# Kernel optimization log

Hardware: AMD Instinct MI355X
Metric: run time of the kernel (lower is better)

## Reference

```python
import jax, jax.numpy as jnp
import numpy as np

BLOCK = 256


def setup_inputs() -> dict:
    key = jax.random.key(0)
    ks = jax.random.split(key, 6)
    b, n, hid = 2, 4096, 2048
    h, d = 16, 128
    x = jax.random.normal(ks[0], (b, n, hid), dtype=jnp.float32)
    slope_rate = jax.random.uniform(ks[1], (h, 1, 1), dtype=jnp.float32)
    Wqkv = jax.random.normal(ks[2], (3 * h * d, hid), dtype=jnp.float32) * 0.02
    Wg = jax.random.normal(ks[3], (h * d, hid), dtype=jnp.float32) * 0.02
    norm_w = jnp.ones((h * d,), dtype=jnp.float32)
    Wo = jax.random.normal(ks[4], (hid, h * d), dtype=jnp.float32) * 0.02
    return {"x": x, "slope_rate": slope_rate, "Wqkv": Wqkv, "Wg": Wg, "norm_w": norm_w, "Wo": Wo}


def reference(x, slope_rate, Wqkv, Wg, norm_w, Wo):
    b, n, hid = x.shape
    h = slope_rate.shape[0]
    d = Wqkv.shape[0] // (3 * h)
    nb = n // BLOCK

    qkv = jax.nn.silu(x @ Wqkv.T).reshape(b, n, h, 3 * d)
    q, k, v = jnp.split(qkv, 3, axis=-1)           # each (b, n, h, d)
    # -> (b, h, n, d)
    q = q.transpose(0, 2, 1, 3)
    k = k.transpose(0, 2, 1, 3)
    v = v.transpose(0, 2, 1, 3)

    s = slope_rate.astype(jnp.float32)             # (h, 1, 1)
    arr = jnp.arange(1, BLOCK + 1, dtype=jnp.float32)
    q_decay = jnp.exp(-s * arr[:, None])           # (h, BLOCK, 1)
    k_decay = jnp.exp(-s * (BLOCK - arr[:, None])) # (h, BLOCK, 1)
    idx = arr[:, None] - arr[None, :]              # (BLOCK, BLOCK)
    diag_decay = jnp.where(idx >= 0, jnp.exp(-s * idx), 0.0)  # (h, BLOCK, BLOCK)
    block_decay = jnp.exp(-s * BLOCK)              # (h, 1, 1)

    # chunk into blocks: (nb, b, h, BLOCK, d)
    def chunk(t):
        return t.reshape(b, h, nb, BLOCK, d).transpose(2, 0, 1, 3, 4)
    qc, kc, vc = chunk(q), chunk(k), chunk(v)

    def step(kv, qkv_blk):
        qi, ki, vi = qkv_blk
        # inter-block: decayed query against running kv state
        out_nd = jnp.einsum('bhmd,bhde->bhme', qi * q_decay, kv)
        # intra-block: decay-masked quadratic attention
        qk = jnp.einsum('bhmd,bhnd->bhmn', qi, ki) * diag_decay
        out_d = jnp.einsum('bhmn,bhne->bhme', qk, vi)
        kv_new = block_decay * kv + jnp.einsum('bhmd,bhme->bhde', ki * k_decay, vi)
        return kv_new, out_nd + out_d

    kv0 = jnp.zeros((b, h, d, d), dtype=jnp.float32)
    _, out_blocks = jax.lax.scan(step, kv0, (qc, kc, vc))  # (nb, b, h, BLOCK, d)

    out = out_blocks.transpose(1, 2, 0, 3, 4).reshape(b, h, n, d)
    out = out.transpose(0, 2, 1, 3).reshape(b, n, h * d)  # b n (h d)

    # RMSNorm
    eps = jnp.finfo(jnp.float32).eps
    rms = jax.lax.rsqrt(jnp.mean(out * out, axis=-1, keepdims=True) + eps)
    out = out * rms * norm_w

    gate = jax.nn.sigmoid(x @ Wg.T)
    return (gate * out) @ Wo.T
```

## Files before the change

### kernel.cpp

```cpp
#include <hip/hip_runtime.h>
#include <stdint.h>

typedef __attribute__((ext_vector_type(8))) short short8;
typedef __attribute__((ext_vector_type(4))) float f32x4;

#define DEV static __device__ __forceinline__

DEV float b2f(unsigned short u) {
  unsigned x = ((unsigned)u) << 16;
  return __builtin_bit_cast(float, x);
}
DEV unsigned short f2b(float f) {
  unsigned x = __builtin_bit_cast(unsigned, f);
  return (unsigned short)((x + 0x7fffu + ((x >> 16) & 1u)) >> 16);
}
DEV void gload16(const unsigned short* g, unsigned short* l) {
  __builtin_amdgcn_global_load_lds((const __attribute__((address_space(1))) void*)g,
                                   (__attribute__((address_space(3))) void*)l, 16, 0, 0);
}
#define MFMA(a, b, c) __builtin_amdgcn_mfma_f32_16x16x32_bf16(a, b, c, 0, 0, 0)
#define BARRIER                          \
  asm volatile("" ::: "memory");         \
  __builtin_amdgcn_s_barrier();          \
  asm volatile("" ::: "memory")

__global__ void k_f2b(const float* __restrict__ in, unsigned short* __restrict__ out, long n) {
  long i = ((long)blockIdx.x * blockDim.x + threadIdx.x) * 4;
  long stride = (long)gridDim.x * blockDim.x * 4;
  for (; i < n; i += stride) {
    float4 f = *(const float4*)(in + i);
    ushort4 o;
    o.x = f2b(f.x); o.y = f2b(f.y); o.z = f2b(f.z); o.w = f2b(f.w);
    *(ushort4*)(out + i) = o;
  }
}

template <int MODE>
__global__ __launch_bounds__(512, 2) void k_gemm(
    const unsigned short* __restrict__ A, const unsigned short* __restrict__ B0,
    const unsigned short* __restrict__ B1,
    unsigned short* __restrict__ o_q, unsigned short* __restrict__ o_k,
    unsigned short* __restrict__ o_v, unsigned short* __restrict__ o_g,
    float* __restrict__ o_f) {
  const int K = 2048, NT = 32;
  __shared__ unsigned short sm[65536];
  int tid = threadIdx.x, w = tid >> 6, lane = tid & 63;
  int wm = w >> 2, wn = w & 3;
  int l15 = lane & 15, l4 = lane >> 4;
  int xcd = blockIdx.x & 7, sub = blockIdx.x >> 3;
  int tm = xcd * 4 + (sub & 3), tn = sub >> 2;
  int brow = tm << 8, bcol = tn << 8;
  const unsigned short* Ab = A + (size_t)brow * K;
  const unsigned short* Bb = (MODE == 1 || bcol < 6144) ? (B0 + (size_t)bcol * K)
                                                        : (B1 + (size_t)(bcol - 6144) * K);
  f32x4 acc[8][4];
#pragma unroll
  for (int m = 0; m < 8; m++)
#pragma unroll
    for (int n = 0; n < 4; n++) acc[m][n] = (f32x4)0.f;

  int rdA[4][2], rdB[4][2];
  const int bslot = (wn >> 1) ? 3 : 1;
  const int bposb = (wn & 1) * 64;
#pragma unroll
  for (int fi = 0; fi < 4; ++fi) {
#pragma unroll
    for (int ks = 0; ks < 2; ++ks) {
      int posA = wm * 64 + fi * 16 + l15;
      rdA[fi][ks] = posA * 128 + (((ks * 4 + l4) ^ (posA & 7)) << 4);
      int posB = bposb + fi * 16 + l15;
      rdB[fi][ks] = bslot * 16384 + posB * 128 + (((ks * 4 + l4) ^ (posB & 7)) << 4);
    }
  }
  const unsigned short* gP[4][2];
  int dL[4][2];
#pragma unroll
  for (int s = 0; s < 4; ++s) {
#pragma unroll
    for (int i = 0; i < 2; ++i) {
      int c = i * 512 + tid;
      int pos = c >> 3, pb = c & 7;
      const unsigned short* gb = (s & 1) ? Bb : Ab;
      int ro = (s >> 1) << 7;
      gP[s][i] = gb + (size_t)(ro + pos) * K + ((pb ^ (pos & 7)) << 3);
      dL[s][i] = s * 16384 + c * 16;
    }
  }

  auto stage = [&](int s, int tgl) {
#pragma unroll
    for (int i = 0; i < 2; ++i) {
      gload16(gP[s][i], (unsigned short*)((char*)sm + (dL[s][i] + tgl)));
      gP[s][i] += 64;
    }
  };

  stage(0, 0); stage(1, 0); stage(3, 0); stage(2, 0);
  asm volatile("s_waitcnt vmcnt(2)" ::: "memory");
  BARRIER;

  for (int T = 0; T < NT; ++T) {
    const char* smb = (const char*)sm + ((T & 1) << 16);
    int tglS = ((T + 1) & 1) << 16;
    short8 af[4][2], bfr[4][2];
#pragma unroll
    for (int nj = 0; nj < 4; ++nj)
#pragma unroll
      for (int ks = 0; ks < 2; ++ks) bfr[nj][ks] = *(const short8*)(smb + rdB[nj][ks]);
#pragma unroll
    for (int fi = 0; fi < 4; ++fi)
#pragma unroll
      for (int ks = 0; ks < 2; ++ks) af[fi][ks] = *(const short8*)(smb + rdA[fi][ks]);
    stage(0, tglS); stage(1, tglS); stage(3, tglS);
    __builtin_amdgcn_s_setprio(1);
#pragma unroll
    for (int mi = 0; mi < 4; ++mi)
#pragma unroll
      for (int nj = 0; nj < 4; ++nj)
#pragma unroll
        for (int ks = 0; ks < 2; ++ks) acc[mi][nj] = MFMA(af[mi][ks], bfr[nj][ks], acc[mi][nj]);
    __builtin_amdgcn_s_setprio(0);
    asm volatile("s_waitcnt vmcnt(6)" ::: "memory");
    BARRIER;
#pragma unroll
    for (int fi = 0; fi < 4; ++fi)
#pragma unroll
      for (int ks = 0; ks < 2; ++ks)
        af[fi][ks] = *(const short8*)(smb + (rdA[fi][ks] + 32768));
    stage(2, tglS);
    __builtin_amdgcn_s_setprio(1);
#pragma unroll
    for (int mi = 0; mi < 4; ++mi)
#pragma unroll
      for (int nj = 0; nj < 4; ++nj)
#pragma unroll
        for (int ks = 0; ks < 2; ++ks)
          acc[4 + mi][nj] = MFMA(af[mi][ks], bfr[nj][ks], acc[4 + mi][nj]);
    __builtin_amdgcn_s_setprio(0);
    asm volatile("s_waitcnt vmcnt(2)" ::: "memory");
    BARRIER;
  }
  asm volatile("s_waitcnt vmcnt(0)" ::: "memory");
  BARRIER;

  if (MODE == 0) {
#pragma unroll
    for (int mf = 0; mf < 8; ++mf) {
      int rowb = (mf >> 2) * 128 + wm * 64 + (mf & 3) * 16 + l4 * 4;
#pragma unroll
      for (int ni = 0; ni < 4; ++ni) {
        int cx = wn * 64 + ((ni ^ l4) << 4) + l15;
        int colg = bcol + wn * 64 + ni * 16 + l15;
#pragma unroll
        for (int r = 0; r < 4; ++r) {
          float v = acc[mf][ni][r];
          float a = (colg < 6144) ? v / (1.f + __expf(-v))
                                  : 1.f / (1.f + __expf(-v));
          sm[(rowb + r) * 256 + cx] = f2b(a);
        }
      }
    }
    BARRIER;
    int rl0 = tid >> 5;
    int ch = (tid & 31) * 8;
    int cg = bcol + ch;
    unsigned short* qkvb = nullptr;
    size_t hbase = 0;
    int off = 0;
    const bool isq = (MODE == 0) && (cg < 6144);
    if (isq) {
      int hh = cg / 384, dd = cg - hh * 384;
      int sel = dd >> 7;
      off = dd & 127;
      qkvb = (sel == 0) ? o_q : (sel == 1) ? o_k : o_v;
      hbase = (size_t)hh * 4096;
    }
#pragma unroll
    for (int it = 0; it < 16; ++it) {
      int rl = it * 16 + rl0;
      int cx = ch ^ (((rl >> 2) & 3) << 4);
      short8 v8 = *(const short8*)(sm + rl * 256 + cx);
      int row = brow + rl;
      if (isq) {
        int b = row >> 12, t = row & 4095;
        *(short8*)(qkvb + ((size_t)b * 65536 + hbase + t) * 128 + off) = v8;
      } else {
        *(short8*)(o_g + (size_t)row * 2048 + (cg - 6144)) = v8;
      }
    }
  } else {
#pragma unroll
    for (int mf = 0; mf < 8; ++mf)
#pragma unroll
      for (int r = 0; r < 4; ++r) {
        int row = brow + (mf >> 2) * 128 + wm * 64 + (mf & 3) * 16 + l4 * 4 + r;
#pragma unroll
        for (int ni = 0; ni < 4; ++ni) {
          int col = bcol + wn * 64 + ni * 16 + l15;
          o_f[(size_t)row * 2048 + col] = acc[mf][ni][r];
        }
      }
  }
}

__global__ __launch_bounds__(256) void k_kvblk(const unsigned short* __restrict__ kk,
                                               const unsigned short* __restrict__ vv,
                                               const float* __restrict__ slope,
                                               unsigned short* __restrict__ kvT) {
  int gid = blockIdx.x;
  int bh = gid >> 4, blk = gid & 15;
  float s = slope[bh & 15];
  __shared__ unsigned short kT[128][72];
  __shared__ unsigned short vT[128][72];
  int tid = threadIdx.x, w = tid >> 6, lane = tid & 63;
  int wrow = (w >> 1) * 64, wcol = (w & 1) * 64;
  f32x4 acc[4][4];
#pragma unroll
  for (int m = 0; m < 4; m++)
#pragma unroll
    for (int n = 0; n < 4; n++) acc[m][n] = (f32x4)0.f;
  const unsigned short* kb = kk + ((size_t)bh * 4096 + blk * 256) * 128;
  const unsigned short* vb = vv + ((size_t)bh * 4096 + blk * 256) * 128;
  int tt = tid & 63, c0 = (tid >> 6) * 32;
  for (int tc = 0; tc < 4; ++tc) {
    __syncthreads();
    int tg = tc * 64 + tt;
    float kd = __expf(-s * (float)(255 - tg));
#pragma unroll
    for (int g = 0; g < 4; ++g) {
      int c = c0 + g * 8;
      short8 k8 = *(const short8*)(kb + (size_t)tg * 128 + c);
      short8 v8 = *(const short8*)(vb + (size_t)tg * 128 + c);
#pragma unroll
      for (int j = 0; j < 8; ++j) {
        kT[c + j][tt] = f2b(b2f((unsigned short)k8[j]) * kd);
        vT[c + j][tt] = (unsigned short)v8[j];
      }
    }
    __syncthreads();
#pragma unroll
    for (int kx = 0; kx < 64; kx += 32) {
      int ko = kx + (lane >> 4) * 8;
      short8 af[4], bfr[4];
#pragma unroll
      for (int m = 0; m < 4; m++) af[m] = *(const short8*)&vT[wrow + m * 16 + (lane & 15)][ko];
#pragma unroll
      for (int n = 0; n < 4; n++) bfr[n] = *(const short8*)&kT[wcol + n * 16 + (lane & 15)][ko];
#pragma unroll
      for (int m = 0; m < 4; m++)
#pragma unroll
        for (int n = 0; n < 4; n++) acc[m][n] = MFMA(af[m], bfr[n], acc[m][n]);
    }
  }
  unsigned short* op = kvT + (size_t)gid * 16384;
#pragma unroll
  for (int m = 0; m < 4; m++)
#pragma unroll
    for (int r = 0; r < 4; r++) {
      int e = wrow + m * 16 + (lane >> 4) * 4 + r;
#pragma unroll
      for (int n = 0; n < 4; n++) {
        int d = wcol + n * 16 + (lane & 15);
        op[e * 128 + d] = f2b(acc[m][n][r]);
      }
    }
}

__global__ void k_scan(unsigned short* kvT, const float* __restrict__ slope) {
  int gid = blockIdx.x;
  int bh = gid >> 6;
  int eo = (gid & 63) * 256 + threadIdx.x;
  float s = slope[bh & 15];
  float bd = __expf(-s * 256.f);
  float st = 0.f;
  size_t base = (size_t)bh * 16 * 16384 + eo;
#pragma unroll
  for (int i = 0; i < 16; ++i) {
    unsigned short c = kvT[base + (size_t)i * 16384];
    kvT[base + (size_t)i * 16384] = f2b(st);
    st = bd * st + b2f(c);
  }
}

__global__ __launch_bounds__(256) void k_attn(const unsigned short* __restrict__ q,
                                              const unsigned short* __restrict__ kk,
                                              const unsigned short* __restrict__ vv,
                                              const unsigned short* __restrict__ kvT,
                                              const float* __restrict__ slope,
                                              unsigned short* __restrict__ attn) {
  int gid = blockIdx.x;
  int hf = gid & 1, blk = (gid >> 1) & 15, bh = gid >> 5;
  float s = slope[bh & 15];
  __shared__ unsigned short k_sh[64][136];
  __shared__ unsigned short vT_sh[128][72];
  __shared__ unsigned short s_sh[4][32][72];
  int tid = threadIdx.x, w = tid >> 6, lane = tid & 63;
  int mm0 = hf * 128 + w * 32;
  const unsigned short* qb = q + ((size_t)bh * 4096 + blk * 256) * 128;
  const unsigned short* kvb = kvT + (size_t)(bh * 16 + blk) * 16384;
  f32x4 acc[2][8];
#pragma unroll
  for (int m = 0; m < 2; m++)
#pragma unroll
    for (int n = 0; n < 8; n++) acc[m][n] = (f32x4)0.f;
#pragma unroll
  for (int kx = 0; kx < 128; kx += 32) {
    int ko = kx + (lane >> 4) * 8;
    short8 af[2], bfr[8];
#pragma unroll
    for (int mi = 0; mi < 2; mi++)
      af[mi] = *(const short8*)(qb + (size_t)(mm0 + mi * 16 + (lane & 15)) * 128 + ko);
#pragma unroll
    for (int ni = 0; ni < 8; ni++)
      bfr[ni] = *(const short8*)(kvb + (size_t)(ni * 16 + (lane & 15)) * 128 + ko);
#pragma unroll
    for (int mi = 0; mi < 2; mi++)
#pragma unroll
      for (int ni = 0; ni < 8; ni++) acc[mi][ni] = MFMA(af[mi], bfr[ni], acc[mi][ni]);
  }
#pragma unroll
  for (int mi = 0; mi < 2; mi++)
#pragma unroll
    for (int r = 0; r < 4; r++) {
      float qd = __expf(-s * (float)(mm0 + mi * 16 + (lane >> 4) * 4 + r + 1));
#pragma unroll
      for (int ni = 0; ni < 8; ni++) acc[mi][ni][r] *= qd;
    }
  int nchunk = 2 * (hf + 1);
  for (int tc = 0; tc < nchunk; ++tc) {
    __syncthreads();
    {
      int t2 = tid >> 2, c = (tid & 3) * 32;
      const unsigned short* kp = kk + ((size_t)bh * 4096 + blk * 256 + tc * 64 + t2) * 128 + c;
#pragma unroll
      for (int g = 0; g < 4; ++g) *(short8*)&k_sh[t2][c + g * 8] = *(const short8*)(kp + g * 8);
    }
    {
      int t2 = tid & 63, e0 = (tid >> 6) * 32;
      const unsigned short* vp = vv + ((size_t)bh * 4096 + blk * 256 + tc * 64 + t2) * 128 + e0;
#pragma unroll
      for (int g = 0; g < 4; ++g) {
        short8 v8 = *(const short8*)(vp + g * 8);
#pragma unroll
        for (int j = 0; j < 8; ++j) vT_sh[e0 + g * 8 + j][t2] = (unsigned short)v8[j];
      }
    }
    __syncthreads();
    if (tc * 64 <= mm0 + 31) {
      f32x4 sa[2][4];
#pragma unroll
      for (int m = 0; m < 2; m++)
#pragma unroll
        for (int n = 0; n < 4; n++) sa[m][n] = (f32x4)0.f;
#pragma unroll
      for (int kx = 0; kx < 128; kx += 32) {
        int ko = kx + (lane >> 4) * 8;
        short8 af[2], bfr[4];
#pragma unroll
        for (int mi = 0; mi < 2; mi++)
          af[mi] = *(const short8*)(qb + (size_t)(mm0 + mi * 16 + (lane & 15)) * 128 + ko);
#pragma unroll
        for (int ni = 0; ni < 4; ni++) bfr[ni] = *(const short8*)&k_sh[ni * 16 + (lane & 15)][ko];
#pragma unroll
        for (int mi = 0; mi < 2; mi++)
#pragma unroll
          for (int ni = 0; ni < 4; ni++) sa[mi][ni] = MFMA(af[mi], bfr[ni], sa[mi][ni]);
      }
#pragma unroll
      for (int mi = 0; mi < 2; mi++)
#pragma unroll
        for (int ni = 0; ni < 4; ni++)
#pragma unroll
          for (int r = 0; r < 4; r++) {
            int mm = mm0 + mi * 16 + (lane >> 4) * 4 + r;
            int ttg = tc * 64 + ni * 16 + (lane & 15);
            int diff = mm - ttg;
            float val = (diff >= 0) ? sa[mi][ni][r] * __expf(-s * (float)diff) : 0.f;
            s_sh[w][mi * 16 + (lane >> 4) * 4 + r][ni * 16 + (lane & 15)] = f2b(val);
          }
#pragma unroll
      for (int k2 = 0; k2 < 64; k2 += 32) {
        int ko2 = k2 + (lane >> 4) * 8;
        short8 a2[2];
#pragma unroll
        for (int mi = 0; mi < 2; mi++)
          a2[mi] = *(const short8*)&s_sh[w][mi * 16 + (lane & 15)][ko2];
#pragma unroll
        for (int ni = 0; ni < 8; ni++) {
          short8 b2 = *(const short8*)&vT_sh[ni * 16 + (lane & 15)][ko2];
#pragma unroll
          for (int mi = 0; mi < 2; mi++) acc[mi][ni] = MFMA(a2[mi], b2, acc[mi][ni]);
        }
      }
    }
  }
  int b = bh >> 4, h = bh & 15;
#pragma unroll
  for (int mi = 0; mi < 2; mi++)
#pragma unroll
    for (int r = 0; r < 4; r++) {
      int mm = mm0 + mi * 16 + (lane >> 4) * 4 + r;
      size_t rowp = ((size_t)b * 4096 + blk * 256 + mm) * 2048 + h * 128;
#pragma unroll
      for (int ni = 0; ni < 8; ni++) attn[rowp + ni * 16 + (lane & 15)] = f2b(acc[mi][ni][r]);
    }
}

__global__ __launch_bounds__(256) void k_norm(const unsigned short* __restrict__ attn,
                                              const unsigned short* __restrict__ gate,
                                              const float* __restrict__ nw,
                                              unsigned short* __restrict__ y) {
  int row = blockIdx.x;
  int tid = threadIdx.x, w = tid >> 6, lane = tid & 63;
  const unsigned short* ap = attn + (size_t)row * 2048 + tid * 8;
  const unsigned short* gp = gate + (size_t)row * 2048 + tid * 8;
  short8 a8 = *(const short8*)ap;
  float vals[8];
  float ss = 0.f;
#pragma unroll
  for (int j = 0; j < 8; ++j) {
    vals[j] = b2f((unsigned short)a8[j]);
    ss += vals[j] * vals[j];
  }
#pragma unroll
  for (int off = 32; off > 0; off >>= 1) ss += __shfl_down(ss, off, 64);
  __shared__ float red[4];
  if (lane == 0) red[w] = ss;
  __syncthreads();
  float tot = red[0] + red[1] + red[2] + red[3];
  float rms = rsqrtf(tot * (1.f / 2048.f) + 1.1920929e-07f);
  short8 g8 = *(const short8*)gp;
  short8 o;
#pragma unroll
  for (int j = 0; j < 8; ++j)
    o[j] = (short)f2b(vals[j] * rms * nw[tid * 8 + j] * b2f((unsigned short)g8[j]));
  *(short8*)(y + (size_t)row * 2048 + tid * 8) = o;
}

extern "C" void kernel_launch(void* const* d_in, const int* in_sizes, int n_in, void* d_out,
                              int out_size, void* d_ws, size_t ws_size, hipStream_t stream) {
  const float* x = (const float*)d_in[0];
  const float* slope = (const float*)d_in[1];
  const float* Wqkv = (const float*)d_in[2];
  const float* Wg = (const float*)d_in[3];
  const float* nw = (const float*)d_in[4];
  const float* Wo = (const float*)d_in[5];
  float* out = (float*)d_out;

  unsigned short* q = (unsigned short*)d_ws;
  unsigned short* k = q + 16777216;
  unsigned short* v = k + 16777216;
  unsigned short* gate = v + 16777216;
  unsigned short* xb = gate + 16777216;
  unsigned short* wqkvb = xb + 16777216;
  unsigned short* wgb = wqkvb + 12582912;
  unsigned short* wob = wgb + 4194304;
  unsigned short* kvT = wob + 4194304;
  unsigned short* attn = wqkvb;
  unsigned short* y = xb;

  k_f2b<<<2048, 256, 0, stream>>>(x, xb, 16777216L);
  k_f2b<<<2048, 256, 0, stream>>>(Wqkv, wqkvb, 12582912L);
  k_f2b<<<1024, 256, 0, stream>>>(Wg, wgb, 4194304L);
  k_f2b<<<1024, 256, 0, stream>>>(Wo, wob, 4194304L);

  k_gemm<0><<<1024, 512, 0, stream>>>(xb, wqkvb, wgb, q, k, v, gate, nullptr);
  k_kvblk<<<512, 256, 0, stream>>>(k, v, slope, kvT);
  k_scan<<<2048, 256, 0, stream>>>(kvT, slope);
  k_attn<<<1024, 256, 0, stream>>>(q, k, v, kvT, slope, attn);
  k_norm<<<8192, 256, 0, stream>>>(attn, gate, nw, y);
  k_gemm<1><<<256, 512, 0, stream>>>(y, wob, nullptr, nullptr, nullptr, nullptr, nullptr, out);
}
```

Before: 454.5 us.

## Merge fp32-to-bf16 conversions into one launch and triple-buffer GEMM K-tiles

Replaces the four separate fp32-to-bf16 conversion launches with a single kernel that converts x and all three weights into one contiguous bf16 buffer, removing launch overhead and tail effects. The GEMM main loop changes from double-buffered 64-wide K tiles, split into two half-stages, to triple-buffered 32-wide K tiles with a simpler rotation, using one barrier per iteration instead of two. Prefetch now runs two tiles ahead, but each iteration does half as many MFMAs between barriers, which may expose more synchronization overhead.

```diff
diff --git a/kernel.cpp b/kernel.cpp
--- a/kernel.cpp
+++ b/kernel.cpp
@@ -24,15 +24,22 @@
   __builtin_amdgcn_s_barrier();          \
   asm volatile("" ::: "memory")
 
-__global__ void k_f2b(const float* __restrict__ in, unsigned short* __restrict__ out, long n) {
-  long i = ((long)blockIdx.x * blockDim.x + threadIdx.x) * 4;
-  long stride = (long)gridDim.x * blockDim.x * 4;
-  for (; i < n; i += stride) {
-    float4 f = *(const float4*)(in + i);
-    ushort4 o;
-    o.x = f2b(f.x); o.y = f2b(f.y); o.z = f2b(f.z); o.w = f2b(f.w);
-    *(ushort4*)(out + i) = o;
-  }
+__global__ __launch_bounds__(256) void k_f2b4(const float* __restrict__ x,
+                                              const float* __restrict__ wqkv,
+                                              const float* __restrict__ wg,
+                                              const float* __restrict__ wo,
+                                              unsigned short* __restrict__ dst) {
+  long gi = ((long)blockIdx.x * 256 + threadIdx.x) * 4;
+  const float* src;
+  long off;
+  if (gi < 16777216L) { src = x; off = gi; }
+  else if (gi < 29360128L) { src = wqkv; off = gi - 16777216L; }
+  else if (gi < 33554432L) { src = wg; off = gi - 29360128L; }
+  else { src = wo; off = gi - 33554432L; }
+  float4 f = *(const float4*)(src + off);
+  ushort4 o;
+  o.x = f2b(f.x); o.y = f2b(f.y); o.z = f2b(f.z); o.w = f2b(f.w);
+  *(ushort4*)(dst + gi) = o;
 }
 
 template <int MODE>
@@ -42,7 +49,7 @@
     unsigned short* __restrict__ o_q, unsigned short* __restrict__ o_k,
     unsigned short* __restrict__ o_v, unsigned short* __restrict__ o_g,
     float* __restrict__ o_f) {
-  const int K = 2048, NT = 32;
+  const int K = 2048, NT = 64;
   __shared__ unsigned short sm[65536];
   int tid = threadIdx.x, w = tid >> 6, lane = tid & 63;
   int wm = w >> 2, wn = w & 3;
@@ -59,86 +66,66 @@
 #pragma unroll
     for (int n = 0; n < 4; n++) acc[m][n] = (f32x4)0.f;
 
-  int rdA[4][2], rdB[4][2];
-  const int bslot = (wn >> 1) ? 3 : 1;
+  int rdA[4], rdB[4];
+  const int bslotb = (wn >> 1) ? 24576 : 8192;
   const int bposb = (wn & 1) * 64;
 #pragma unroll
   for (int fi = 0; fi < 4; ++fi) {
-#pragma unroll
-    for (int ks = 0; ks < 2; ++ks) {
-      int posA = wm * 64 + fi * 16 + l15;
-      rdA[fi][ks] = posA * 128 + (((ks * 4 + l4) ^ (posA & 7)) << 4);
-      int posB = bposb + fi * 16 + l15;
-      rdB[fi][ks] = bslot * 16384 + posB * 128 + (((ks * 4 + l4) ^ (posB & 7)) << 4);
-    }
-  }
-  const unsigned short* gP[4][2];
-  int dL[4][2];
-#pragma unroll
-  for (int s = 0; s < 4; ++s) {
-#pragma unroll
-    for (int i = 0; i < 2; ++i) {
-      int c = i * 512 + tid;
-      int pos = c >> 3, pb = c & 7;
+    int posA = wm * 64 + fi * 16 + l15;
+    rdA[fi] = posA * 64 + ((l4 ^ (posA & 3)) << 4);
+    int posB = bposb + fi * 16 + l15;
+    rdB[fi] = bslotb + posB * 64 + ((l4 ^ (posB & 3)) << 4);
+  }
+  const unsigned short* gP[4];
+  {
+    int pos = tid >> 2, pb = tid & 3;
+    int scol = (pb ^ (pos & 3)) << 3;
+#pragma unroll
+    for (int s = 0; s < 4; ++s) {
       const unsigned short* gb = (s & 1) ? Bb : Ab;
       int ro = (s >> 1) << 7;
-      gP[s][i] = gb + (size_t)(ro + pos) * K + ((pb ^ (pos & 7)) << 3);
-      dL[s][i] = s * 16384 + c * 16;
-    }
-  }
-
-  auto stage = [&](int s, int tgl) {
-#pragma unroll
-    for (int i = 0; i < 2; ++i) {
-      gload16(gP[s][i], (unsigned short*)((char*)sm + (dL[s][i] + tgl)));
-      gP[s][i] += 64;
+      gP[s] = gb + (size_t)(ro + pos) * K + scol;
+    }
+  }
+  const int dLb = tid * 16;
+
+  auto stage = [&](int bufbyte) {
+#pragma unroll
+    for (int s = 0; s < 4; ++s) {
+      gload16(gP[s], (unsigned short*)((char*)sm + bufbyte + s * 8192 + dLb));
+      gP[s] += 32;
     }
   };
 
-  stage(0, 0); stage(1, 0); stage(3, 0); stage(2, 0);
-  asm volatile("s_waitcnt vmcnt(2)" ::: "memory");
+  stage(0);
+  stage(32768);
+  asm volatile("s_waitcnt vmcnt(4)" ::: "memory");
   BARRIER;
 
+  int b0 = 0, b1 = 32768, b2 = 65536;
   for (int T = 0; T < NT; ++T) {
-    const char* smb = (const char*)sm + ((T & 1) << 16);
-    int tglS = ((T + 1) & 1) << 16;
-    short8 af[4][2], bfr[4][2];
-#pragma unroll
-    for (int nj = 0; nj < 4; ++nj)
-#pragma unroll
-      for (int ks = 0; ks < 2; ++ks) bfr[nj][ks] = *(const short8*)(smb + rdB[nj][ks]);
-#pragma unroll
-    for (int fi = 0; fi < 4; ++fi)
-#pragma unroll
-      for (int ks = 0; ks < 2; ++ks) af[fi][ks] = *(const short8*)(smb + rdA[fi][ks]);
-    stage(0, tglS); stage(1, tglS); stage(3, tglS);
+    stage(b2);
+    const char* smb = (const char*)sm + b0;
+    short8 bfr[4], afA[4], afB[4];
+#pragma unroll
+    for (int nj = 0; nj < 4; ++nj) bfr[nj] = *(const short8*)(smb + rdB[nj]);
+#pragma unroll
+    for (int fi = 0; fi < 4; ++fi) afA[fi] = *(const short8*)(smb + rdA[fi]);
+#pragma unroll
+    for (int fi = 0; fi < 4; ++fi) afB[fi] = *(const short8*)(smb + (rdA[fi] + 16384));
     __builtin_amdgcn_s_setprio(1);
 #pragma unroll
     for (int mi = 0; mi < 4; ++mi)
 #pragma unroll
-      for (int nj = 0; nj < 4; ++nj)
-#pragma unroll
-        for (int ks = 0; ks < 2; ++ks) acc[mi][nj] = MFMA(af[mi][ks], bfr[nj][ks], acc[mi][nj]);
+      for (int nj = 0; nj < 4; ++nj) acc[mi][nj] = MFMA(afA[mi], bfr[nj], acc[mi][nj]);
+#pragma unroll
+    for (int mi = 0; mi < 4; ++mi)
+#pragma unroll
+      for (int nj = 0; nj < 4; ++nj) acc[4 + mi][nj] = MFMA(afB[mi], bfr[nj], acc[4 + mi][nj]);
     __builtin_amdgcn_s_setprio(0);
-    asm volatile("s_waitcnt vmcnt(6)" ::: "memory");
+    asm volatile("s_waitcnt vmcnt(4)" ::: "memory");
     BARRIER;
-#pragma unroll
-    for (int fi = 0; fi < 4; ++fi)
-#pragma unroll
-      for (int ks = 0; ks < 2; ++ks)
-        af[fi][ks] = *(const short8*)(smb + (rdA[fi][ks] + 32768));
-    stage(2, tglS);
-    __builtin_amdgcn_s_setprio(1);
-#pragma unroll
-    for (int mi = 0; mi < 4; ++mi)
-#pragma unroll
-      for (int nj = 0; nj < 4; ++nj)
-#pragma unroll
-        for (int ks = 0; ks < 2; ++ks)
-          acc[4 + mi][nj] = MFMA(af[mi][ks], bfr[nj][ks], acc[4 + mi][nj]);
-    __builtin_amdgcn_s_setprio(0);
-    asm volatile("s_waitcnt vmcnt(2)" ::: "memory");
-    BARRIER;
+    int t = b0; b0 = b1; b1 = b2; b2 = t;
   }
   asm volatile("s_waitcnt vmcnt(0)" ::: "memory");
   BARRIER;
@@ -167,7 +154,7 @@
     unsigned short* qkvb = nullptr;
     size_t hbase = 0;
     int off = 0;
-    const bool isq = (MODE == 0) && (cg < 6144);
+    const bool isq = (cg < 6144);
     if (isq) {
       int hh = cg / 384, dd = cg - hh * 384;
       int sel = dd >> 7;
@@ -459,10 +446,7 @@
   unsigned short* attn = wqkvb;
   unsigned short* y = xb;
 
-  k_f2b<<<2048, 256, 0, stream>>>(x, xb, 16777216L);
-  k_f2b<<<2048, 256, 0, stream>>>(Wqkv, wqkvb, 12582912L);
-  k_f2b<<<1024, 256, 0, stream>>>(Wg, wgb, 4194304L);
-  k_f2b<<<1024, 256, 0, stream>>>(Wo, wob, 4194304L);
+  k_f2b4<<<36864, 256, 0, stream>>>(x, Wqkv, Wg, Wo, xb);
 
   k_gemm<0><<<1024, 512, 0, stream>>>(xb, wqkvb, wgb, q, k, v, gate, nullptr);
   k_kvblk<<<512, 256, 0, stream>>>(k, v, slope, kvT);
```

New measurement: 481.8 us. +6.0%, slower.
